# Kernel tuning notes

Hardware: AMD Instinct MI355X
Metric: run time of the kernel (lower is better)

Reference implementation:

```python
import jax, jax.numpy as jnp
import numpy as np

B, L, D = 64, 256, 768
LABELS = 200
REL_OFF = 256  # to_pos[k] = k + 256


def setup_inputs() -> dict:
    key = jax.random.key(0)
    ks = jax.random.split(key, 8)
    return {
        "sequence_output": jax.random.normal(ks[0], (B, L, D), dtype=jnp.float32),
        "pos_embedding": jax.random.normal(ks[1], (2 * REL_OFF + 1, D), dtype=jnp.float32) * 0.02,
        "class_embedding": jax.random.normal(ks[2], (LABELS + 1, D), dtype=jnp.float32) * 0.02,
        "W": jax.random.normal(ks[3], (LABELS, 3 * D), dtype=jnp.float32) * 0.02,
        "b": jnp.zeros((LABELS,), dtype=jnp.float32),
        "head_indexes": jax.random.randint(ks[4], (B, L), 0, L),
        "frame": jax.random.randint(ks[5], (B,), 0, LABELS + 1),
        "pos": jax.random.randint(ks[6], (B,), 0, L),
    }


def reference(sequence_output, pos_embedding, class_embedding, W, b, head_indexes, frame, pos):
    # per-batch gather of token rows: sequence_output[i] = sequence_output[i][head_indexes[i]]
    gathered = jnp.take_along_axis(sequence_output, head_indexes[:, :, None], axis=1)  # [B,L,D]

    j = jnp.arange(sequence_output.shape[1])  # [L]
    rel = j[None, :] - pos[:, None] + REL_OFF  # [B,L] in [0, 512]
    pe = pos_embedding[rel]  # [B,L,D]

    # frame embedding only at j == pos[i], else class_embedding[0]
    fe_hit = class_embedding[frame]  # [B,D]
    is_pos = (j[None, :] == pos[:, None])[:, :, None]  # [B,L,1]
    fe = jnp.where(is_pos, fe_hit[:, None, :], class_embedding[0][None, None, :])  # [B,L,D]

    feat = jnp.concatenate([gathered, pe, fe], axis=-1)  # [B,L,3D]
    # dropout is identity at inference; classifier linear
    return jnp.einsum("blf,cf->blc", feat, W) + b
```

## Files before the change

### kernel.cpp

```cpp
#include <hip/hip_runtime.h>
#include <stdint.h>


typedef __attribute__((ext_vector_type(8))) short short8;
typedef __attribute__((ext_vector_type(4))) float f32x4;

#define AS1 __attribute__((address_space(1)))
#define AS3 __attribute__((address_space(3)))

#define NSEQ_G 1572864
#define NPE_G  49248
#define NCE_G  19296
#define NW16_G 73728
#define SEQB_OFF 0
#define PEB_OFF  12582912
#define CEB_OFF  (PEB_OFF + 393984)
#define WP_OFF   (CEB_OFF + 154368)
#define WS_ELEMS (WP_OFF + 589824)
#define WS_NEED  ((size_t)WS_ELEMS * 2)
#define TILE_STRIDE 36864

__device__ __forceinline__ unsigned short f2bf(float f) {
    union { float f; unsigned int u; } v; v.f = f;
    unsigned int u = v.u;
    return (unsigned short)((u + 0x7fffu + ((u >> 16) & 1u)) >> 16);
}

__device__ __forceinline__ short8 pack8(f32x4 a, f32x4 b) {
    short8 r;
    r[0] = (short)f2bf(a.x); r[1] = (short)f2bf(a.y);
    r[2] = (short)f2bf(a.z); r[3] = (short)f2bf(a.w);
    r[4] = (short)f2bf(b.x); r[5] = (short)f2bf(b.y);
    r[6] = (short)f2bf(b.z); r[7] = (short)f2bf(b.w);
    return r;
}

__device__ __forceinline__ void dma16(const unsigned short* g, AS3 unsigned short* l) {
    __builtin_amdgcn_global_load_lds((AS1 const unsigned int*)g,
                                     (AS3 unsigned int*)l, 16, 0, 0);
}

__global__ void prep_kernel(const float* __restrict__ seq,
                            const float* __restrict__ pe,
                            const float* __restrict__ ce,
                            const float* __restrict__ W,
                            unsigned short* __restrict__ ws) {
    int g = blockIdx.x * 256 + threadIdx.x;
    if (g < NSEQ_G) {
        const float* p = seq + (size_t)g * 8;
        *(short8*)(ws + SEQB_OFF + (size_t)g * 8) =
            pack8(*(const f32x4*)p, *(const f32x4*)(p + 4));
        return;
    }
    g -= NSEQ_G;
    if (g < NPE_G) {
        const float* p = pe + (size_t)g * 8;
        *(short8*)(ws + PEB_OFF + (size_t)g * 8) =
            pack8(*(const f32x4*)p, *(const f32x4*)(p + 4));
        return;
    }
    g -= NPE_G;
    if (g < NCE_G) {
        const float* p = ce + (size_t)g * 8;
        *(short8*)(ws + CEB_OFF + (size_t)g * 8) =
            pack8(*(const f32x4*)p, *(const f32x4*)(p + 4));
        return;
    }
    g -= NCE_G;
    if (g < NW16_G) {
        int n   = g & 15;
        int kb8 = (g >> 4) % 288;
        int t   = g / (288 * 16);
        int row = t * 16 + n;
        int col = kb8 * 8;
        f32x4 a = {0.f, 0.f, 0.f, 0.f}, b = {0.f, 0.f, 0.f, 0.f};
        if (row < 200) {
            const float* p = W + (size_t)row * 2304 + col;
            a = *(const f32x4*)p;
            b = *(const f32x4*)(p + 4);
        }
        *(short8*)(ws + WP_OFF + (size_t)g * 8) = pack8(a, b);
    }
}

__global__ __launch_bounds__(512) void gemm6_kernel(
    const unsigned short* __restrict__ ws,
    const float* __restrict__ bias,
    const int*   __restrict__ head,
    const int*   __restrict__ frame,
    const int*   __restrict__ pos,
    float* __restrict__ out)
{
    __shared__ unsigned short lds[8192 + 16384];

    const unsigned short* seqb = ws + SEQB_OFF;
    const unsigned short* peb  = ws + PEB_OFF;
    const unsigned short* ceb  = ws + CEB_OFF;
    const unsigned short* Wp   = ws + WP_OFF;

    const int tid  = threadIdx.x;
    const int wave = tid >> 6;
    const int lane = tid & 63;
    const int n16  = lane & 15;
    const int quad = lane >> 4;

    const int mblk = blockIdx.x & 255;
    const int h    = blockIdx.x >> 8;

    const int i       = mblk >> 2;
    const int pos_i   = pos[i];
    const int frame_i = frame[i];

    const int smf = wave & 3;
    const int skb = (wave >> 2) * 2;
    const int srow = mblk * 64 + smf * 16 + n16;
    const unsigned short* aSt[3];
    {
        const int sj   = srow & 255;
        const int shi  = head[srow];
        const int srel = sj - pos_i + 256;
        const int scls = (sj == pos_i) ? frame_i : 0;
        const int loff = quad * 8;
        aSt[0] = seqb + ((size_t)i * 256 + (size_t)shi) * 768 + loff;
        aSt[1] = peb + (size_t)srel * 768 + loff;
        aSt[2] = ceb + (size_t)scls * 768 + loff;
    }
    AS3 unsigned short* aDst0 =
        (AS3 unsigned short*)lds + ((smf * 4 + skb) * 64 + lane) * 8;
    AS3 unsigned short* aDst1 = aDst0 + 512;

    const unsigned short* bSt = Wp + (size_t)(h * 8 + wave) * TILE_STRIDE + lane * 8;
    AS3 unsigned short* bDst =
        (AS3 unsigned short*)lds + 8192 + wave * 2048 + lane * 8;

    const int p = wave & 1;
    const int q = wave >> 1;

    const unsigned short* aRd[2];
    const unsigned short* bRd[2];
#pragma unroll
    for (int f = 0; f < 2; ++f)
        aRd[f] = lds + (2 * p + f) * 2048 + lane * 8;
#pragma unroll
    for (int u = 0; u < 2; ++u)
        bRd[u] = lds + 8192 + (q + 4 * u) * 2048 + quad * 128 + n16 * 8;

    f32x4 acc[2][2];
#pragma unroll
    for (int u = 0; u < 2; ++u) {
        const int col = (h * 8 + q + 4 * u) * 16 + n16;
        const float bv = (col < 200) ? bias[col] : 0.0f;
        acc[0][u] = (f32x4){bv, bv, bv, bv};
        acc[1][u] = (f32x4){bv, bv, bv, bv};
    }

#pragma unroll
    for (int sg = 0; sg < 3; ++sg) {
        const unsigned short* aSrc = aSt[sg];
        const unsigned short* bSrc = bSt + (size_t)sg * 12288;
        for (int cc = 0; cc < 6; ++cc) {
            dma16(aSrc + cc * 128 + skb * 32,      aDst0);
            dma16(aSrc + cc * 128 + skb * 32 + 32, aDst1);
            dma16(bSrc + cc * 2048,        bDst);
            dma16(bSrc + cc * 2048 + 512,  bDst + 512);
            dma16(bSrc + cc * 2048 + 1024, bDst + 1024);
            dma16(bSrc + cc * 2048 + 1536, bDst + 1536);
            __syncthreads();
#pragma unroll
            for (int ks = 0; ks < 4; ++ks) {
                short8 a0 = *(const short8*)(aRd[0] + ks * 512);
                short8 a1 = *(const short8*)(aRd[1] + ks * 512);
#pragma unroll
                for (int u = 0; u < 2; ++u) {
                    short8 bf = *(const short8*)(bRd[u] + ks * 512);
                    acc[0][u] = __builtin_amdgcn_mfma_f32_16x16x32_bf16(a0, bf, acc[0][u], 0, 0, 0);
                    acc[1][u] = __builtin_amdgcn_mfma_f32_16x16x32_bf16(a1, bf, acc[1][u], 0, 0, 0);
                }
            }
            __syncthreads();
        }
    }

#pragma unroll
    for (int f = 0; f < 2; ++f) {
        const int rbase = mblk * 64 + (2 * p + f) * 16 + quad * 4;
#pragma unroll
        for (int u = 0; u < 2; ++u) {
            const int col = (h * 8 + q + 4 * u) * 16 + n16;
            if (col < 200) {
#pragma unroll
                for (int r = 0; r < 4; ++r)
                    out[(size_t)(rbase + r) * 200 + col] = acc[f][u][r];
            }
        }
    }
}

__global__ __launch_bounds__(256) void gemm_fallback(
    const float* __restrict__ seq, const float* __restrict__ pe,
    const float* __restrict__ ce, const float* __restrict__ Wf,
    const float* __restrict__ bias, const int* __restrict__ head,
    const int* __restrict__ frame, const int* __restrict__ pos,
    float* __restrict__ out)
{
    const int tid  = threadIdx.x;
    const int wave = tid >> 6;
    const int lane = tid & 63;
    const int n16  = lane & 15;
    const int quad = lane >> 4;

    const int mrow  = blockIdx.x * 16 + n16;
    const int i     = mrow >> 8;
    const int j     = mrow & 255;
    const int pos_i = pos[i];
    const int hi    = head[mrow];
    const int rel   = j - pos_i + 256;
    const int cls   = (j == pos_i) ? frame[i] : 0;

    const float* segs[3];
    segs[0] = seq + ((size_t)i * 256 + (size_t)hi) * 768 + quad * 8;
    segs[1] = pe + (size_t)rel * 768 + quad * 8;
    segs[2] = ce + (size_t)cls * 768 + quad * 8;

    const int ntl = (wave == 0) ? 4 : 3;
    f32x4 acc[4];
#pragma unroll
    for (int u = 0; u < 4; ++u) {
        const int t = wave + 4 * u;
        const int col = t * 16 + n16;
        const float bv = (t < 13 && col < 200) ? bias[col] : 0.0f;
        acc[u] = (f32x4){bv, bv, bv, bv};
    }

    for (int s = 0; s < 3; ++s) {
        const float* ap = segs[s];
#pragma unroll 2
        for (int kk = 0; kk < 768; kk += 32) {
            short8 afr = pack8(*(const f32x4*)(ap + kk), *(const f32x4*)(ap + kk + 4));
#pragma unroll
            for (int u = 0; u < 4; ++u) {
                if (u < ntl) {
                    const int t = wave + 4 * u;
                    const int row = t * 16 + n16;
                    short8 bfr = {0, 0, 0, 0, 0, 0, 0, 0};
                    if (row < 200) {
                        const float* qp = Wf + (size_t)row * 2304 + s * 768 + kk + quad * 8;
                        bfr = pack8(*(const f32x4*)qp, *(const f32x4*)(qp + 4));
                    }
                    acc[u] = __builtin_amdgcn_mfma_f32_16x16x32_bf16(afr, bfr, acc[u], 0, 0, 0);
                }
            }
        }
    }

    const int rbase = blockIdx.x * 16 + quad * 4;
#pragma unroll
    for (int u = 0; u < 4; ++u) {
        const int t = wave + 4 * u;
        if (t < 13) {
            const int col = t * 16 + n16;
            if (col < 200) {
#pragma unroll
                for (int r = 0; r < 4; ++r)
                    out[(size_t)(rbase + r) * 200 + col] = acc[u][r];
            }
        }
    }
}

extern "C" void kernel_launch(void* const* d_in, const int* in_sizes, int n_in,
                              void* d_out, int out_size, void* d_ws, size_t ws_size,
                              hipStream_t stream) {
    const float* seq  = (const float*)d_in[0];
    const float* pe   = (const float*)d_in[1];
    const float* ce   = (const float*)d_in[2];
    const float* W    = (const float*)d_in[3];
    const float* bias = (const float*)d_in[4];
    const int* head   = (const int*)d_in[5];
    const int* frame  = (const int*)d_in[6];
    const int* pos    = (const int*)d_in[7];
    float* out = (float*)d_out;

    if (d_ws != nullptr && ws_size >= WS_NEED) {
        unsigned short* ws = (unsigned short*)d_ws;
        const int total_g = NSEQ_G + NPE_G + NCE_G + NW16_G;
        prep_kernel<<<(total_g + 255) / 256, 256, 0, stream>>>(seq, pe, ce, W, ws);
        gemm6_kernel<<<512, 512, 0, stream>>>(ws, bias, head, frame, pos, out);
    } else {
        gemm_fallback<<<1024, 256, 0, stream>>>(seq, pe, ce, W, bias, head,
                                                frame, pos, out);
    }
}
```

Before: 129.7 us.

## Fuse fp32-to-bf16 activation conversion into GEMM via fp32 LDS staging

The pre-pass that converted the whole sequence, positional and class tables to bf16 in workspace is removed, and only W is still converted up front. The GEMM now DMAs fp32 activation rows directly into LDS and packs them to bf16 just before each MFMA. This avoids writing and re-reading a roughly 25 MB bf16 copy of the sequence tensor. The cost is twice the LDS traffic and footprint for A tiles, extra conversion ALU work in the inner loop, and A being read from global once per column-half block (twice total) in fp32.

```diff
diff --git a/kernel.cpp b/kernel.cpp
--- a/kernel.cpp
+++ b/kernel.cpp
@@ -8,16 +8,8 @@
 #define AS1 __attribute__((address_space(1)))
 #define AS3 __attribute__((address_space(3)))
 
-#define NSEQ_G 1572864
-#define NPE_G  49248
-#define NCE_G  19296
 #define NW16_G 73728
-#define SEQB_OFF 0
-#define PEB_OFF  12582912
-#define CEB_OFF  (PEB_OFF + 393984)
-#define WP_OFF   (CEB_OFF + 154368)
-#define WS_ELEMS (WP_OFF + 589824)
-#define WS_NEED  ((size_t)WS_ELEMS * 2)
+#define WP_NEED ((size_t)589824 * 2)
 #define TILE_STRIDE 36864
 
 __device__ __forceinline__ unsigned short f2bf(float f) {
@@ -39,64 +31,42 @@
     __builtin_amdgcn_global_load_lds((AS1 const unsigned int*)g,
                                      (AS3 unsigned int*)l, 16, 0, 0);
 }
-
-__global__ void prep_kernel(const float* __restrict__ seq,
-                            const float* __restrict__ pe,
-                            const float* __restrict__ ce,
-                            const float* __restrict__ W,
-                            unsigned short* __restrict__ ws) {
+__device__ __forceinline__ void dma16f(const float* g, AS3 float* l) {
+    __builtin_amdgcn_global_load_lds((AS1 const unsigned int*)g,
+                                     (AS3 unsigned int*)l, 16, 0, 0);
+}
+
+__global__ void cvt_w_kernel(const float* __restrict__ W,
+                             unsigned short* __restrict__ Wp) {
     int g = blockIdx.x * 256 + threadIdx.x;
-    if (g < NSEQ_G) {
-        const float* p = seq + (size_t)g * 8;
-        *(short8*)(ws + SEQB_OFF + (size_t)g * 8) =
-            pack8(*(const f32x4*)p, *(const f32x4*)(p + 4));
-        return;
-    }
-    g -= NSEQ_G;
-    if (g < NPE_G) {
-        const float* p = pe + (size_t)g * 8;
-        *(short8*)(ws + PEB_OFF + (size_t)g * 8) =
-            pack8(*(const f32x4*)p, *(const f32x4*)(p + 4));
-        return;
-    }
-    g -= NPE_G;
-    if (g < NCE_G) {
-        const float* p = ce + (size_t)g * 8;
-        *(short8*)(ws + CEB_OFF + (size_t)g * 8) =
-            pack8(*(const f32x4*)p, *(const f32x4*)(p + 4));
-        return;
-    }
-    g -= NCE_G;
-    if (g < NW16_G) {
-        int n   = g & 15;
-        int kb8 = (g >> 4) % 288;
-        int t   = g / (288 * 16);
-        int row = t * 16 + n;
-        int col = kb8 * 8;
-        f32x4 a = {0.f, 0.f, 0.f, 0.f}, b = {0.f, 0.f, 0.f, 0.f};
-        if (row < 200) {
-            const float* p = W + (size_t)row * 2304 + col;
-            a = *(const f32x4*)p;
-            b = *(const f32x4*)(p + 4);
-        }
-        *(short8*)(ws + WP_OFF + (size_t)g * 8) = pack8(a, b);
-    }
-}
-
-__global__ __launch_bounds__(512) void gemm6_kernel(
-    const unsigned short* __restrict__ ws,
+    if (g >= NW16_G) return;
+    int n   = g & 15;
+    int kb8 = (g >> 4) % 288;
+    int t   = g / (288 * 16);
+    int row = t * 16 + n;
+    int col = kb8 * 8;
+    f32x4 a = {0.f, 0.f, 0.f, 0.f}, b = {0.f, 0.f, 0.f, 0.f};
+    if (row < 200) {
+        const float* p = W + (size_t)row * 2304 + col;
+        a = *(const f32x4*)p;
+        b = *(const f32x4*)(p + 4);
+    }
+    *(short8*)(Wp + (size_t)g * 8) = pack8(a, b);
+}
+
+__global__ __launch_bounds__(512) void gemm7_kernel(
+    const float* __restrict__ seq,
+    const float* __restrict__ pe,
+    const float* __restrict__ ce,
     const float* __restrict__ bias,
     const int*   __restrict__ head,
     const int*   __restrict__ frame,
     const int*   __restrict__ pos,
+    const unsigned short* __restrict__ Wp,
     float* __restrict__ out)
 {
-    __shared__ unsigned short lds[8192 + 16384];
-
-    const unsigned short* seqb = ws + SEQB_OFF;
-    const unsigned short* peb  = ws + PEB_OFF;
-    const unsigned short* ceb  = ws + CEB_OFF;
-    const unsigned short* Wp   = ws + WP_OFF;
+    __shared__ float          ldsA[8192];
+    __shared__ unsigned short ldsB[16384];
 
     const int tid  = threadIdx.x;
     const int wave = tid >> 6;
@@ -114,36 +84,30 @@
     const int smf = wave & 3;
     const int skb = (wave >> 2) * 2;
     const int srow = mblk * 64 + smf * 16 + n16;
-    const unsigned short* aSt[3];
+    const float* aSt[3];
     {
         const int sj   = srow & 255;
         const int shi  = head[srow];
         const int srel = sj - pos_i + 256;
         const int scls = (sj == pos_i) ? frame_i : 0;
-        const int loff = quad * 8;
-        aSt[0] = seqb + ((size_t)i * 256 + (size_t)shi) * 768 + loff;
-        aSt[1] = peb + (size_t)srel * 768 + loff;
-        aSt[2] = ceb + (size_t)scls * 768 + loff;
-    }
-    AS3 unsigned short* aDst0 =
-        (AS3 unsigned short*)lds + ((smf * 4 + skb) * 64 + lane) * 8;
-    AS3 unsigned short* aDst1 = aDst0 + 512;
+        aSt[0] = seq + ((size_t)i * 256 + (size_t)shi) * 768 + quad * 4;
+        aSt[1] = pe + (size_t)srel * 768 + quad * 4;
+        aSt[2] = ce + (size_t)scls * 768 + quad * 4;
+    }
+    AS3 float* aD[2][2];
+#pragma unroll
+    for (int e = 0; e < 2; ++e)
+#pragma unroll
+        for (int hh = 0; hh < 2; ++hh)
+            aD[e][hh] = (AS3 float*)ldsA +
+                        ((smf * 4 + skb + e) * 512 + hh * 256 + lane * 4);
 
     const unsigned short* bSt = Wp + (size_t)(h * 8 + wave) * TILE_STRIDE + lane * 8;
-    AS3 unsigned short* bDst =
-        (AS3 unsigned short*)lds + 8192 + wave * 2048 + lane * 8;
+    AS3 unsigned short* bD = (AS3 unsigned short*)ldsB + wave * 2048 + lane * 8;
 
     const int p = wave & 1;
     const int q = wave >> 1;
-
-    const unsigned short* aRd[2];
-    const unsigned short* bRd[2];
-#pragma unroll
-    for (int f = 0; f < 2; ++f)
-        aRd[f] = lds + (2 * p + f) * 2048 + lane * 8;
-#pragma unroll
-    for (int u = 0; u < 2; ++u)
-        bRd[u] = lds + 8192 + (q + 4 * u) * 2048 + quad * 128 + n16 * 8;
+    const int aoff = (quad >> 1) * 256 + (quad & 1) * 128 + n16 * 4;
 
     f32x4 acc[2][2];
 #pragma unroll
@@ -156,25 +120,34 @@
 
 #pragma unroll
     for (int sg = 0; sg < 3; ++sg) {
-        const unsigned short* aSrc = aSt[sg];
+        const float* aSrc = aSt[sg];
         const unsigned short* bSrc = bSt + (size_t)sg * 12288;
         for (int cc = 0; cc < 6; ++cc) {
-            dma16(aSrc + cc * 128 + skb * 32,      aDst0);
-            dma16(aSrc + cc * 128 + skb * 32 + 32, aDst1);
-            dma16(bSrc + cc * 2048,        bDst);
-            dma16(bSrc + cc * 2048 + 512,  bDst + 512);
-            dma16(bSrc + cc * 2048 + 1024, bDst + 1024);
-            dma16(bSrc + cc * 2048 + 1536, bDst + 1536);
+#pragma unroll
+            for (int e = 0; e < 2; ++e)
+#pragma unroll
+                for (int hh = 0; hh < 2; ++hh)
+                    dma16f(aSrc + cc * 128 + (skb + e) * 32 + hh * 16, aD[e][hh]);
+#pragma unroll
+            for (int r = 0; r < 4; ++r)
+                dma16(bSrc + cc * 2048 + r * 512, bD + r * 512);
             __syncthreads();
 #pragma unroll
             for (int ks = 0; ks < 4; ++ks) {
-                short8 a0 = *(const short8*)(aRd[0] + ks * 512);
-                short8 a1 = *(const short8*)(aRd[1] + ks * 512);
+                short8 af[2];
+#pragma unroll
+                for (int f = 0; f < 2; ++f) {
+                    const float* ap = ldsA + ((2 * p + f) * 4 + ks) * 512 + aoff;
+                    f32x4 v0 = *(const f32x4*)ap;
+                    f32x4 v1 = *(const f32x4*)(ap + 64);
+                    af[f] = pack8(v0, v1);
+                }
 #pragma unroll
                 for (int u = 0; u < 2; ++u) {
-                    short8 bf = *(const short8*)(bRd[u] + ks * 512);
-                    acc[0][u] = __builtin_amdgcn_mfma_f32_16x16x32_bf16(a0, bf, acc[0][u], 0, 0, 0);
-                    acc[1][u] = __builtin_amdgcn_mfma_f32_16x16x32_bf16(a1, bf, acc[1][u], 0, 0, 0);
+                    short8 bf = *(const short8*)(ldsB + (q + 4 * u) * 2048 +
+                                                 ks * 512 + quad * 128 + n16 * 8);
+                    acc[0][u] = __builtin_amdgcn_mfma_f32_16x16x32_bf16(af[0], bf, acc[0][u], 0, 0, 0);
+                    acc[1][u] = __builtin_amdgcn_mfma_f32_16x16x32_bf16(af[1], bf, acc[1][u], 0, 0, 0);
                 }
             }
             __syncthreads();
@@ -281,11 +254,11 @@
     const int* pos    = (const int*)d_in[7];
     float* out = (float*)d_out;
 
-    if (d_ws != nullptr && ws_size >= WS_NEED) {
-        unsigned short* ws = (unsigned short*)d_ws;
-        const int total_g = NSEQ_G + NPE_G + NCE_G + NW16_G;
-        prep_kernel<<<(total_g + 255) / 256, 256, 0, stream>>>(seq, pe, ce, W, ws);
-        gemm6_kernel<<<512, 512, 0, stream>>>(ws, bias, head, frame, pos, out);
+    if (d_ws != nullptr && ws_size >= WP_NEED) {
+        unsigned short* Wp = (unsigned short*)d_ws;
+        cvt_w_kernel<<<(NW16_G + 255) / 256, 256, 0, stream>>>(W, Wp);
+        gemm7_kernel<<<512, 512, 0, stream>>>(seq, pe, ce, bias, head, frame,
+                                              pos, Wp, out);
     } else {
         gemm_fallback<<<1024, 256, 0, stream>>>(seq, pe, ce, W, bias, head,
                                                 frame, pos, out);
```

After: 142.8 us. +10.1%, slower.
